# Kernel tuning notes

Measured on AMD Instinct MI355X. Metric: run time of the kernel, lower is better.

## Reference

```python
import jax, jax.numpy as jnp
import numpy as np

WIN = 25            # window size (win_h == win_w == 25)
DIM = 256           # channels
DIM_HEAD = 32
HEADS = DIM // DIM_HEAD   # 8
HIDDEN = int(DIM * 2.0)   # mlp_ratio = 2.0
EPS = 1e-5


def _rel_pos_indices(w=WIN):
    # replicates the buffer built in Attention.__init__
    pos = np.arange(w)
    gi, gj = np.meshgrid(pos, pos, indexing='ij')
    grid = np.stack([gi.ravel(), gj.ravel()], axis=-1)          # (w*w, 2)
    rel = grid[:, None, :] - grid[None, :, :] + (w - 1)          # (n, n, 2)
    return jnp.asarray(rel[..., 0] * (2 * w - 1) + rel[..., 1])  # (n, n) int


def setup_inputs() -> dict:
    key = jax.random.key(0)
    ks = jax.random.split(key, 8)
    s = 0.02
    d = DIM
    return {
        'x': jax.random.normal(ks[0], (2, d, 100, 100), jnp.float32),
        'w_qkv': jax.random.normal(ks[1], (3 * d, d), jnp.float32) * s,
        'w_out': jax.random.normal(ks[2], (d, d), jnp.float32) * s,
        'rel_bias_table': jax.random.normal(ks[3], ((2 * WIN - 1) ** 2, HEADS), jnp.float32) * s,
        'gamma2': jnp.ones((d,), jnp.float32),
        'beta2': jnp.zeros((d,), jnp.float32),
        'w1': jax.random.normal(ks[4], (HIDDEN, d), jnp.float32) * s,
        'b1': jnp.zeros((HIDDEN,), jnp.float32),
        'w2': jax.random.normal(ks[5], (d, HIDDEN), jnp.float32) * s,
        'b2': jnp.zeros((d,), jnp.float32),
    }


def _layernorm(x, g, b, eps=EPS):
    m = x.mean(-1, keepdims=True)
    v = ((x - m) ** 2).mean(-1, keepdims=True)
    return (x - m) / jnp.sqrt(v + eps) * g + b


def reference(x, w_qkv, w_out, rel_bias_table, gamma2, beta2, w1, b1, w2, b2):
    b, d, H, W = x.shape
    nh, nw = H // WIN, W // WIN
    h, dh = HEADS, DIM_HEAD
    scale = dh ** -0.5
    n = WIN * WIN

    # --- window partition: (b, d, H, W) -> (b*nh*nw, n, d) ---
    xw = x.reshape(b, d, nh, WIN, nw, WIN).transpose(0, 2, 4, 3, 5, 1)
    xw = xw.reshape(b * nh * nw, n, d)

    # --- windowed attention with relative-position bias (norm1 unused in source) ---
    qkv = xw @ w_qkv.T                         # (B, n, 3d)
    q, k, v = jnp.split(qkv, 3, axis=-1)
    split_heads = lambda t: t.reshape(t.shape[0], n, h, dh).transpose(0, 2, 1, 3)
    q = split_heads(q) * scale                 # (B, h, n, dh)
    k = split_heads(k)
    v = split_heads(v)

    sim = jnp.einsum('bhid,bhjd->bhij', q, k)  # (B, h, n, n)
    bias = rel_bias_table[_rel_pos_indices()]  # (n, n, h)
    sim = sim + bias.transpose(2, 0, 1)[None]
    attn = jax.nn.softmax(sim, axis=-1)
    out = jnp.einsum('bhij,bhjd->bhid', attn, v)            # (B, h, n, dh)
    out = out.transpose(0, 2, 1, 3).reshape(-1, n, d)        # head-major concat: (m d)
    out = out @ w_out.T                                      # (B, n, d)

    # --- un-partition: (b*nh*nw, n, d) -> (b, d, H, W) ---
    xa = out.reshape(b, nh, nw, WIN, WIN, d).transpose(0, 5, 1, 3, 2, 4)
    xa = xa.reshape(b, d, H, W)

    # --- norm2 + MLP + residual ---
    y = xa.transpose(0, 2, 3, 1).reshape(b, H * W, d)
    y = _layernorm(y, gamma2, beta2)
    y = jax.nn.gelu(y @ w1.T + b1, approximate=False) @ w2.T + b2
    y = y.reshape(b, H, W, d).transpose(0, 3, 1, 2)
    return x + y
```

## Files before the change

kernel.cpp:

```cpp
#include <hip/hip_runtime.h>


using f32x4 = __attribute__((ext_vector_type(4))) float;
using s16x8 = __attribute__((ext_vector_type(8))) short;

__device__ __forceinline__ ushort f2b(float f) {
  union { float f; unsigned u; } v; v.f = f;
  return (ushort)((v.u + 0x7FFFu + ((v.u >> 16) & 1u)) >> 16);
}
__device__ __forceinline__ ushort f2b_fast(float f) {
  union { float f; unsigned u; } v; v.f = f;
  return (ushort)((v.u + 0x8000u) >> 16);
}
__device__ __forceinline__ float b2f(ushort u) {
  union { unsigned u; float f; } v; v.u = ((unsigned)u) << 16; return v.f;
}
__device__ __forceinline__ float lo2f(unsigned w) {
  union { unsigned u; float f; } v; v.u = w << 16; return v.f;
}
__device__ __forceinline__ float hi2f(unsigned w) {
  union { unsigned u; float f; } v; v.u = w & 0xffff0000u; return v.f;
}

__device__ __forceinline__ void gld16(const void* g, void* l) {
  __builtin_amdgcn_global_load_lds((const __attribute__((address_space(1))) void*)g,
                                   (__attribute__((address_space(3))) void*)l, 16, 0, 0);
}

template<int KB>
__device__ __forceinline__ void gemm_core(const ushort* __restrict__ A, int lda,
                                          const ushort* __restrict__ B, int ldb,
                                          f32x4 acc[4][4]) {
  __shared__ ushort As[128 * 64];
  __shared__ ushort Bs[128 * 64];
  const int tid = threadIdx.x;
  const int lane = tid & 63;
  const int wv = tid >> 6;
  const int wr = (wv >> 1) * 64;
  const int wc = (wv & 1) * 64;
  const int srow = (lane >> 3);
  const int sg = ((lane & 7) ^ (srow & 7)) * 8;
  f32x4 zero = {0.f, 0.f, 0.f, 0.f};
#pragma unroll
  for (int mt = 0; mt < 4; ++mt)
#pragma unroll
    for (int nt = 0; nt < 4; ++nt) acc[mt][nt] = zero;

  for (int kb = 0; kb < KB; ++kb) {
#pragma unroll
    for (int j = 0; j < 4; ++j) {
      int r0 = wv * 32 + j * 8;
      int row = r0 + srow;
      gld16(A + row * lda + kb * 64 + sg, &As[r0 * 64]);
      gld16(B + row * ldb + kb * 64 + sg, &Bs[r0 * 64]);
    }
    __syncthreads();
#pragma unroll
    for (int ks = 0; ks < 2; ++ks) {
      s16x8 af[4], bfr[4];
      const int G = ks * 4 + (lane >> 4);
#pragma unroll
      for (int mt = 0; mt < 4; ++mt) {
        int row = wr + mt * 16 + (lane & 15);
        af[mt] = *(const s16x8*)&As[row * 64 + (G ^ (row & 7)) * 8];
      }
#pragma unroll
      for (int nt = 0; nt < 4; ++nt) {
        int row = wc + nt * 16 + (lane & 15);
        bfr[nt] = *(const s16x8*)&Bs[row * 64 + (G ^ (row & 7)) * 8];
      }
#pragma unroll
      for (int mt = 0; mt < 4; ++mt)
#pragma unroll
        for (int nt = 0; nt < 4; ++nt)
          acc[mt][nt] = __builtin_amdgcn_mfma_f32_16x16x32_bf16(af[mt], bfr[nt], acc[mt][nt], 0, 0, 0);
    }
    __syncthreads();
  }
}

__global__ __launch_bounds__(256) void k_prep(const float* __restrict__ x,
                                              const float* __restrict__ wqkv,
                                              const float* __restrict__ wout,
                                              const float* __restrict__ w1,
                                              const float* __restrict__ w2,
                                              const float* __restrict__ table,
                                              ushort* __restrict__ Xw,
                                              ushort* __restrict__ wqkvb,
                                              ushort* __restrict__ woutb,
                                              ushort* __restrict__ w1b,
                                              ushort* __restrict__ w2b,
                                              ushort* __restrict__ biasPh) {
  __shared__ ushort smem[64 * 264];
  const int bid = blockIdx.x, tid = threadIdx.x;
  if (bid < 320) {
    ushort (*Ls)[264] = (ushort(*)[264])smem;
    const int t0 = bid * 64;
    const int w = t0 / 640;
    const int tokbase = t0 - w * 640;
    const int b = w >> 4, wh = (w >> 2) & 3, ww = w & 3;
    for (int i = tid; i < 64 * 256; i += 256) {
      int c = i >> 6, tl = i & 63;
      int tok = tokbase + tl;
      ushort val = 0;
      if (tok < 625) {
        int ii = tok / 25, jj = tok - ii * 25;
        val = f2b(x[((b * 256 + c) * 100 + wh * 25 + ii) * 100 + ww * 25 + jj]);
      }
      Ls[tl][c] = val;
    }
    __syncthreads();
    for (int i = tid; i < 64 * 32; i += 256) {
      int tl = i >> 5, g = (i & 31) * 8;
      *(uint4*)(Xw + (t0 + tl) * 256 + g) = *(const uint4*)&Ls[tl][g];
    }
  } else if (bid < 832) {
    int v = (bid - 320) * 1024 + tid * 4;
    const float* src; ushort* dst; int off;
    if (v < 196608)      { src = wqkv; dst = wqkvb; off = v; }
    else if (v < 262144) { src = wout; dst = woutb; off = v - 196608; }
    else if (v < 393216) { src = w1;   dst = w1b;   off = v - 262144; }
    else                 { src = w2;   dst = w2b;   off = v - 393216; }
    float4 f = *(const float4*)(src + off);
    ushort4 u; u.x = f2b(f.x); u.y = f2b(f.y); u.z = f2b(f.z); u.w = f2b(f.w);
    *(ushort4*)(dst + off) = u;
  } else {
    float* tl = (float*)smem;
    const int q = bid - 832;
    const int h = q / 40, t = q - (q / 40) * 40;
    for (int i = tid; i < 2401; i += 256) tl[i] = table[i * 8 + h] * 1.4426950408889634f;
    __syncthreads();
    const int lane = tid >> 2, rr = tid & 3;
    const int quad = lane >> 4, cl = lane & 15;
    int row = t * 16 + quad * 4 + rr;
    int rowg = (row < 625) ? row : 0;
    const int ri = rowg / 25, ci = rowg - ri * 25;
    for (int cc = 0; cc < 4; ++cc)
      for (int cp = 0; cp < 5; ++cp)
#pragma unroll
        for (int codd = 0; codd < 2; ++codd) {
          int col = cc * 160 + (cp * 2 + codd) * 16 + cl;
          float v = -1e30f;
          if (col < 625) {
            int rj = col / 25, cj = col - rj * 25;
            v = tl[(ri - rj + 24) * 49 + (ci - cj + 24)];
          }
          biasPh[((((h * 40 + t) * 4 + cc) * 5 + cp) * 64 + lane) * 8 + codd * 4 + rr] = f2b(v);
        }
  }
}

__global__ __launch_bounds__(256) void k_qkv(const ushort* __restrict__ Xw,
                                             const ushort* __restrict__ Wb,
                                             ushort* __restrict__ Qb,
                                             ushort* __restrict__ Kb,
                                             ushort* __restrict__ Vb) {
  f32x4 acc[4][4];
  gemm_core<4>(Xw + blockIdx.x * 128 * 256, 256, Wb + blockIdx.y * 128 * 256, 256, acc);
  const int lane = threadIdx.x & 63, wv = threadIdx.x >> 6;
  const int wr = (wv >> 1) * 64, wc = (wv & 1) * 64;
  const float QSC = 0.17677669529663687f * 1.4426950408889634f;
#pragma unroll
  for (int mt = 0; mt < 4; ++mt) {
#pragma unroll
    for (int nt = 0; nt < 4; ++nt) {
      int n = blockIdx.y * 128 + wc + nt * 16 + (lane & 15);
      int which = n >> 8, h = (n >> 5) & 7, ch = n & 31;
      ushort* dst = which == 0 ? Qb : (which == 1 ? Kb : Vb);
      float sc = which == 0 ? QSC : 1.f;
#pragma unroll
      for (int r = 0; r < 4; ++r) {
        int m = blockIdx.x * 128 + wr + mt * 16 + (lane >> 4) * 4 + r;
        int w = m / 640, tok = m - w * 640;
        dst[(((w << 3) + h) * 640 + tok) * 32 + ch] = f2b_fast(acc[mt][nt][r] * sc);
      }
    }
  }
}

__global__ __launch_bounds__(256, 2) void k_attn(const ushort* __restrict__ Qb,
                                                 const ushort* __restrict__ Kb,
                                                 const ushort* __restrict__ Vb,
                                                 const ushort* __restrict__ biasPh,
                                                 ushort* __restrict__ AO) {
  __shared__ ushort Vt[32][646];
  __shared__ ushort Pw[4][16][164];
  const int tid = threadIdx.x;
  const int lane = tid & 63;
  const int wv = tid >> 6;
  const int quad = lane >> 4;
  const int cl = lane & 15;
  const int bid = blockIdx.x;
  const int tg = bid % 10;
  const int wh = bid / 10;
  const int h = wh & 7;
  const int win = wh >> 3;
  const ushort* Qg = Qb + (win * 8 + h) * 20480;
  const ushort* Kg = Kb + (win * 8 + h) * 20480;
  const ushort* Vg = Vb + (win * 8 + h) * 20480;

#pragma unroll
  for (int k = 0; k < 10; ++k) {
    int idx = tid + k * 256;
    int tok = idx >> 2, c0 = (idx & 3) * 8;
    ushort tmp[8];
    *(uint4*)tmp = *(const uint4*)(Vg + tok * 32 + c0);
#pragma unroll
    for (int j = 0; j < 8; ++j) Vt[c0 + j][tok] = tmp[j];
  }
  __syncthreads();

  const int t = tg * 4 + wv;
  const s16x8 qf = *(const s16x8*)(Qg + (t * 16 + cl) * 32 + quad * 8);
  const f32x4 zero = {0.f, 0.f, 0.f, 0.f};
  f32x4 o0 = zero, o1 = zero;
  float osum[4] = {0.f, 0.f, 0.f, 0.f};

  for (int cc = 0; cc < 4; ++cc) {
    f32x4 s[10];
#pragma unroll
    for (int c = 0; c < 10; ++c) {
      s16x8 kf = *(const s16x8*)(Kg + (cc * 160 + c * 16 + cl) * 32 + quad * 8);
      s[c] = __builtin_amdgcn_mfma_f32_16x16x32_bf16(qf, kf, zero, 0, 0, 0);
    }
    const ushort* bp = biasPh + (((h * 40 + t) * 4 + cc) * 5) * 512 + lane * 8;
#pragma unroll
    for (int cp = 0; cp < 5; ++cp) {
      s16x8 bb = *(const s16x8*)(bp + cp * 512);
      const unsigned* bw = (const unsigned*)&bb;
#pragma unroll
      for (int codd = 0; codd < 2; ++codd) {
        int c = cp * 2 + codd;
        unsigned w0 = bw[codd * 2], w1 = bw[codd * 2 + 1];
        s[c][0] += lo2f(w0); s[c][1] += hi2f(w0);
        s[c][2] += lo2f(w1); s[c][3] += hi2f(w1);
      }
    }
#pragma unroll
    for (int c = 0; c < 10; ++c)
#pragma unroll
      for (int r = 0; r < 4; ++r) {
        float p = exp2f(s[c][r]);
        osum[r] += p;
        Pw[wv][quad * 4 + r][c * 16 + cl] = f2b_fast(p);
      }
#pragma unroll
    for (int kc = 0; kc < 5; ++kc) {
      s16x8 pf = *(const s16x8*)&Pw[wv][cl][kc * 32 + quad * 8];
      s16x8 vf0 = *(const s16x8*)&Vt[cl][cc * 160 + kc * 32 + quad * 8];
      s16x8 vf1 = *(const s16x8*)&Vt[16 + cl][cc * 160 + kc * 32 + quad * 8];
      o0 = __builtin_amdgcn_mfma_f32_16x16x32_bf16(pf, vf0, o0, 0, 0, 0);
      o1 = __builtin_amdgcn_mfma_f32_16x16x32_bf16(pf, vf1, o1, 0, 0, 0);
    }
  }
#pragma unroll
  for (int r = 0; r < 4; ++r) {
    float ss = osum[r];
    ss += __shfl_xor(ss, 1, 64); ss += __shfl_xor(ss, 2, 64);
    ss += __shfl_xor(ss, 4, 64); ss += __shfl_xor(ss, 8, 64);
    float inv = 1.f / ss;
    int tok = t * 16 + quad * 4 + r;
    if (tok < 625) {
      int base = (win * 640 + tok) * 256 + h * 32;
      AO[base + cl] = f2b_fast(o0[r] * inv);
      AO[base + 16 + cl] = f2b_fast(o1[r] * inv);
    }
  }
}

__global__ __launch_bounds__(256, 2) void k_out_ln(const ushort* __restrict__ AO,
                                                   const ushort* __restrict__ Wb,
                                                   const float* __restrict__ gamma,
                                                   const float* __restrict__ beta,
                                                   ushort* __restrict__ Yn) {
  __shared__ ushort As[128 * 64];
  __shared__ ushort Bs[256 * 64];
  __shared__ float red[2][128][2];
  const int tid = threadIdx.x;
  const int lane = tid & 63;
  const int wv = tid >> 6;
  const int wr = (wv >> 1) * 64, wc = (wv & 1) * 128;
  const int quad = lane >> 4, cl = lane & 15;
  const int srow = lane >> 3;
  const int sg = ((lane & 7) ^ (srow & 7)) * 8;
  f32x4 zero = {0.f, 0.f, 0.f, 0.f};
  f32x4 acc[4][8];
#pragma unroll
  for (int mt = 0; mt < 4; ++mt)
#pragma unroll
    for (int nt = 0; nt < 8; ++nt) acc[mt][nt] = zero;

  const ushort* A = AO + blockIdx.x * 128 * 256;
  for (int kb = 0; kb < 4; ++kb) {
#pragma unroll
    for (int i = 0; i < 12; ++i) {
      int r0 = wv * 8 + i * 32;
      int row = r0 + srow;
      if (r0 < 128) gld16(A + row * 256 + kb * 64 + sg, &As[r0 * 64]);
      else          gld16(Wb + (row - 128) * 256 + kb * 64 + sg, &Bs[(r0 - 128) * 64]);
    }
    __syncthreads();
#pragma unroll
    for (int ks = 0; ks < 2; ++ks) {
      s16x8 af[4], bfr[8];
      const int G = ks * 4 + quad;
#pragma unroll
      for (int mt = 0; mt < 4; ++mt) {
        int row = wr + mt * 16 + cl;
        af[mt] = *(const s16x8*)&As[row * 64 + (G ^ (row & 7)) * 8];
      }
#pragma unroll
      for (int nt = 0; nt < 8; ++nt) {
        int row = wc + nt * 16 + cl;
        bfr[nt] = *(const s16x8*)&Bs[row * 64 + (G ^ (row & 7)) * 8];
      }
#pragma unroll
      for (int mt = 0; mt < 4; ++mt)
#pragma unroll
        for (int nt = 0; nt < 8; ++nt)
          acc[mt][nt] = __builtin_amdgcn_mfma_f32_16x16x32_bf16(af[mt], bfr[nt], acc[mt][nt], 0, 0, 0);
    }
    __syncthreads();
  }
#pragma unroll
  for (int mt = 0; mt < 4; ++mt)
#pragma unroll
    for (int r = 0; r < 4; ++r) {
      float s = 0.f, ss = 0.f;
#pragma unroll
      for (int nt = 0; nt < 8; ++nt) { float v = acc[mt][nt][r]; s += v; ss += v * v; }
      s += __shfl_xor(s, 1, 64); ss += __shfl_xor(ss, 1, 64);
      s += __shfl_xor(s, 2, 64); ss += __shfl_xor(ss, 2, 64);
      s += __shfl_xor(s, 4, 64); ss += __shfl_xor(ss, 4, 64);
      s += __shfl_xor(s, 8, 64); ss += __shfl_xor(ss, 8, 64);
      if (cl == 0) {
        int row = wr + mt * 16 + quad * 4 + r;
        red[wc >> 7][row][0] = s;
        red[wc >> 7][row][1] = ss;
      }
    }
  __syncthreads();
  float g[8], bt[8];
#pragma unroll
  for (int nt = 0; nt < 8; ++nt) { int n = wc + nt * 16 + cl; g[nt] = gamma[n]; bt[nt] = beta[n]; }
  const int m0 = blockIdx.x * 128;
#pragma unroll
  for (int mt = 0; mt < 4; ++mt)
#pragma unroll
    for (int r = 0; r < 4; ++r) {
      int row = wr + mt * 16 + quad * 4 + r;
      int m = m0 + row;
      int w = m / 640, tok = m - w * 640;
      if (tok < 625) {
        float sum = red[0][row][0] + red[1][row][0];
        float ssum = red[0][row][1] + red[1][row][1];
        float mean = sum * 0.00390625f;
        float var = ssum * 0.00390625f - mean * mean;
        float rstd = rsqrtf(var + 1e-5f);
        int b = w >> 4, whh = (w >> 2) & 3, www = w & 3;
        int ii = tok / 25, jj = tok - ii * 25;
        int p = (whh * 25 + ii) * 100 + www * 25 + jj;
        ushort* dst = Yn + (b * 10000 + p) * 256;
#pragma unroll
        for (int nt = 0; nt < 8; ++nt) {
          float v = (acc[mt][nt][r] - mean) * rstd * g[nt] + bt[nt];
          dst[wc + nt * 16 + cl] = f2b_fast(v);
        }
      }
    }
}

__global__ __launch_bounds__(256) void k_fc1(const ushort* __restrict__ Yn,
                                             const ushort* __restrict__ W1b,
                                             const float* __restrict__ b1,
                                             ushort* __restrict__ G) {
  f32x4 acc[4][4];
  gemm_core<4>(Yn + blockIdx.x * 128 * 256, 256, W1b + blockIdx.y * 128 * 256, 256, acc);
  const int lane = threadIdx.x & 63, wv = threadIdx.x >> 6;
  const int wr = (wv >> 1) * 64, wc = (wv & 1) * 64;
#pragma unroll
  for (int mt = 0; mt < 4; ++mt)
#pragma unroll
    for (int nt = 0; nt < 4; ++nt) {
      int n = blockIdx.y * 128 + wc + nt * 16 + (lane & 15);
      float bias = b1[n];
#pragma unroll
      for (int r = 0; r < 4; ++r) {
        int m = blockIdx.x * 128 + wr + mt * 16 + (lane >> 4) * 4 + r;
        float v = acc[mt][nt][r] + bias;
        v = 0.5f * v * (1.f + erff(v * 0.70710678118f));
        G[m * 512 + n] = f2b_fast(v);
      }
    }
}

__global__ __launch_bounds__(256) void k_fc2(const ushort* __restrict__ W2b,
                                             const ushort* __restrict__ G,
                                             const float* __restrict__ b2,
                                             const float* __restrict__ x,
                                             float* __restrict__ out) {
  f32x4 acc[4][4];
  gemm_core<8>(W2b + blockIdx.x * 128 * 512, 512, G + blockIdx.y * 128 * 512, 512, acc);
  const int lane = threadIdx.x & 63, wv = threadIdx.x >> 6;
  const int wr = (wv >> 1) * 64, wc = (wv & 1) * 64;
#pragma unroll
  for (int mt = 0; mt < 4; ++mt)
#pragma unroll
    for (int nt = 0; nt < 4; ++nt) {
      int t = blockIdx.y * 128 + wc + nt * 16 + (lane & 15);
      if (t < 20000) {
        int b = t / 10000, p = t - b * 10000;
#pragma unroll
        for (int r = 0; r < 4; ++r) {
          int c = blockIdx.x * 128 + wr + mt * 16 + (lane >> 4) * 4 + r;
          int idx = (b * 256 + c) * 10000 + p;
          out[idx] = x[idx] + acc[mt][nt][r] + b2[c];
        }
      }
    }
}

extern "C" void kernel_launch(void* const* d_in, const int* in_sizes, int n_in,
                              void* d_out, int out_size, void* d_ws, size_t ws_size,
                              hipStream_t stream) {
  const float* x     = (const float*)d_in[0];
  const float* wqkv  = (const float*)d_in[1];
  const float* wout  = (const float*)d_in[2];
  const float* bias  = (const float*)d_in[3];
  const float* gamma = (const float*)d_in[4];
  const float* beta  = (const float*)d_in[5];
  const float* w1    = (const float*)d_in[6];
  const float* b1    = (const float*)d_in[7];
  const float* w2    = (const float*)d_in[8];
  const float* b2    = (const float*)d_in[9];
  float* out = (float*)d_out;
  char* ws = (char*)d_ws;

  ushort* Xw    = (ushort*)(ws + 0);
  ushort* AO    = Xw;
  ushort* wqkvb = (ushort*)(ws + 10485760);
  ushort* woutb = (ushort*)(ws + 10878976);
  ushort* w1b   = (ushort*)(ws + 11010048);
  ushort* w2b   = (ushort*)(ws + 11272192);
  ushort* Qb    = (ushort*)(ws + 11534336);
  ushort* Kb    = (ushort*)(ws + 22020096);
  ushort* Vb    = (ushort*)(ws + 32505856);
  ushort* biasPh= (ushort*)(ws + 42991616);
  ushort* Yn    = (ushort*)(ws + 22020096);
  ushort* G     = (ushort*)(ws + 32505856);

  k_prep  <<<1152, 256, 0, stream>>>(x, wqkv, wout, w1, w2, bias,
                                     Xw, wqkvb, woutb, w1b, w2b, biasPh);
  k_qkv   <<<dim3(160, 6), 256, 0, stream>>>(Xw, wqkvb, Qb, Kb, Vb);
  k_attn  <<<2560, 256, 0, stream>>>(Qb, Kb, Vb, biasPh, AO);
  k_out_ln<<<160, 256, 0, stream>>>(AO, woutb, gamma, beta, Yn);
  k_fc1   <<<dim3(157, 4), 256, 0, stream>>>(Yn, w1b, b1, G);
  k_fc2   <<<dim3(2, 157), 256, 0, stream>>>(w2b, G, b2, x, out);
}
```

Before: 244.1 us.

## Write V transposed from QKV GEMM, drop LDS transpose in attention, shrink out-proj tile

```diff
diff --git a/kernel.cpp b/kernel.cpp
--- a/kernel.cpp
+++ b/kernel.cpp
@@ -154,36 +154,42 @@
                                              const ushort* __restrict__ Wb,
                                              ushort* __restrict__ Qb,
                                              ushort* __restrict__ Kb,
-                                             ushort* __restrict__ Vb) {
+                                             ushort* __restrict__ VbT) {
   f32x4 acc[4][4];
   gemm_core<4>(Xw + blockIdx.x * 128 * 256, 256, Wb + blockIdx.y * 128 * 256, 256, acc);
   const int lane = threadIdx.x & 63, wv = threadIdx.x >> 6;
   const int wr = (wv >> 1) * 64, wc = (wv & 1) * 64;
+  const int which = blockIdx.y >> 1;
   const float QSC = 0.17677669529663687f * 1.4426950408889634f;
 #pragma unroll
   for (int mt = 0; mt < 4; ++mt) {
 #pragma unroll
     for (int nt = 0; nt < 4; ++nt) {
       int n = blockIdx.y * 128 + wc + nt * 16 + (lane & 15);
-      int which = n >> 8, h = (n >> 5) & 7, ch = n & 31;
-      ushort* dst = which == 0 ? Qb : (which == 1 ? Kb : Vb);
-      float sc = which == 0 ? QSC : 1.f;
-#pragma unroll
-      for (int r = 0; r < 4; ++r) {
-        int m = blockIdx.x * 128 + wr + mt * 16 + (lane >> 4) * 4 + r;
-        int w = m / 640, tok = m - w * 640;
-        dst[(((w << 3) + h) * 640 + tok) * 32 + ch] = f2b_fast(acc[mt][nt][r] * sc);
-      }
-    }
-  }
-}
-
-__global__ __launch_bounds__(256, 2) void k_attn(const ushort* __restrict__ Qb,
+      int h = (n >> 5) & 7, ch = n & 31;
+      int m0 = blockIdx.x * 128 + wr + mt * 16 + (lane >> 4) * 4;
+      int w = m0 / 640, tok0 = m0 - w * 640;
+      if (which == 2) {
+        ushort4 pk;
+        pk.x = f2b_fast(acc[mt][nt][0]); pk.y = f2b_fast(acc[mt][nt][1]);
+        pk.z = f2b_fast(acc[mt][nt][2]); pk.w = f2b_fast(acc[mt][nt][3]);
+        *(ushort4*)(VbT + (((w << 3) + h) * 32 + ch) * 640 + tok0) = pk;
+      } else {
+        ushort* dst = which == 0 ? Qb : Kb;
+        float sc = which == 0 ? QSC : 1.f;
+#pragma unroll
+        for (int r = 0; r < 4; ++r)
+          dst[(((w << 3) + h) * 640 + tok0 + r) * 32 + ch] = f2b_fast(acc[mt][nt][r] * sc);
+      }
+    }
+  }
+}
+
+__global__ __launch_bounds__(256, 4) void k_attn(const ushort* __restrict__ Qb,
                                                  const ushort* __restrict__ Kb,
-                                                 const ushort* __restrict__ Vb,
+                                                 const ushort* __restrict__ VbT,
                                                  const ushort* __restrict__ biasPh,
                                                  ushort* __restrict__ AO) {
-  __shared__ ushort Vt[32][646];
   __shared__ ushort Pw[4][16][164];
   const int tid = threadIdx.x;
   const int lane = tid & 63;
@@ -191,24 +197,13 @@
   const int quad = lane >> 4;
   const int cl = lane & 15;
   const int bid = blockIdx.x;
-  const int tg = bid % 10;
-  const int wh = bid / 10;
-  const int h = wh & 7;
-  const int win = wh >> 3;
+  const int h = bid & 7;
+  const int rem = bid >> 3;
+  const int win = rem / 10;
+  const int tg = rem - win * 10;
   const ushort* Qg = Qb + (win * 8 + h) * 20480;
   const ushort* Kg = Kb + (win * 8 + h) * 20480;
-  const ushort* Vg = Vb + (win * 8 + h) * 20480;
-
-#pragma unroll
-  for (int k = 0; k < 10; ++k) {
-    int idx = tid + k * 256;
-    int tok = idx >> 2, c0 = (idx & 3) * 8;
-    ushort tmp[8];
-    *(uint4*)tmp = *(const uint4*)(Vg + tok * 32 + c0);
-#pragma unroll
-    for (int j = 0; j < 8; ++j) Vt[c0 + j][tok] = tmp[j];
-  }
-  __syncthreads();
+  const ushort* Vt = VbT + (win * 8 + h) * 20480;
 
   const int t = tg * 4 + wv;
   const s16x8 qf = *(const s16x8*)(Qg + (t * 16 + cl) * 32 + quad * 8);
@@ -247,8 +242,8 @@
 #pragma unroll
     for (int kc = 0; kc < 5; ++kc) {
       s16x8 pf = *(const s16x8*)&Pw[wv][cl][kc * 32 + quad * 8];
-      s16x8 vf0 = *(const s16x8*)&Vt[cl][cc * 160 + kc * 32 + quad * 8];
-      s16x8 vf1 = *(const s16x8*)&Vt[16 + cl][cc * 160 + kc * 32 + quad * 8];
+      s16x8 vf0 = *(const s16x8*)(Vt + cl * 640 + cc * 160 + kc * 32 + quad * 8);
+      s16x8 vf1 = *(const s16x8*)(Vt + (16 + cl) * 640 + cc * 160 + kc * 32 + quad * 8);
       o0 = __builtin_amdgcn_mfma_f32_16x16x32_bf16(pf, vf0, o0, 0, 0, 0);
       o1 = __builtin_amdgcn_mfma_f32_16x16x32_bf16(pf, vf1, o1, 0, 0, 0);
     }
@@ -273,39 +268,39 @@
                                                    const float* __restrict__ gamma,
                                                    const float* __restrict__ beta,
                                                    ushort* __restrict__ Yn) {
-  __shared__ ushort As[128 * 64];
+  __shared__ ushort As[64 * 64];
   __shared__ ushort Bs[256 * 64];
-  __shared__ float red[2][128][2];
+  __shared__ float red[2][64][2];
   const int tid = threadIdx.x;
   const int lane = tid & 63;
   const int wv = tid >> 6;
-  const int wr = (wv >> 1) * 64, wc = (wv & 1) * 128;
+  const int wr = (wv >> 1) * 32, wc = (wv & 1) * 128;
   const int quad = lane >> 4, cl = lane & 15;
   const int srow = lane >> 3;
   const int sg = ((lane & 7) ^ (srow & 7)) * 8;
   f32x4 zero = {0.f, 0.f, 0.f, 0.f};
-  f32x4 acc[4][8];
-#pragma unroll
-  for (int mt = 0; mt < 4; ++mt)
+  f32x4 acc[2][8];
+#pragma unroll
+  for (int mt = 0; mt < 2; ++mt)
 #pragma unroll
     for (int nt = 0; nt < 8; ++nt) acc[mt][nt] = zero;
 
-  const ushort* A = AO + blockIdx.x * 128 * 256;
+  const ushort* A = AO + blockIdx.x * 64 * 256;
   for (int kb = 0; kb < 4; ++kb) {
 #pragma unroll
-    for (int i = 0; i < 12; ++i) {
-      int r0 = wv * 8 + i * 32;
+    for (int i = 0; i < 10; ++i) {
+      int r0 = (wv + i * 4) * 8;
       int row = r0 + srow;
-      if (r0 < 128) gld16(A + row * 256 + kb * 64 + sg, &As[r0 * 64]);
-      else          gld16(Wb + (row - 128) * 256 + kb * 64 + sg, &Bs[(r0 - 128) * 64]);
+      if (r0 < 64) gld16(A + row * 256 + kb * 64 + sg, &As[r0 * 64]);
+      else         gld16(Wb + (row - 64) * 256 + kb * 64 + sg, &Bs[(r0 - 64) * 64]);
     }
     __syncthreads();
 #pragma unroll
     for (int ks = 0; ks < 2; ++ks) {
-      s16x8 af[4], bfr[8];
+      s16x8 af[2], bfr[8];
       const int G = ks * 4 + quad;
 #pragma unroll
-      for (int mt = 0; mt < 4; ++mt) {
+      for (int mt = 0; mt < 2; ++mt) {
         int row = wr + mt * 16 + cl;
         af[mt] = *(const s16x8*)&As[row * 64 + (G ^ (row & 7)) * 8];
       }
@@ -315,7 +310,7 @@
         bfr[nt] = *(const s16x8*)&Bs[row * 64 + (G ^ (row & 7)) * 8];
       }
 #pragma unroll
-      for (int mt = 0; mt < 4; ++mt)
+      for (int mt = 0; mt < 2; ++mt)
 #pragma unroll
         for (int nt = 0; nt < 8; ++nt)
           acc[mt][nt] = __builtin_amdgcn_mfma_f32_16x16x32_bf16(af[mt], bfr[nt], acc[mt][nt], 0, 0, 0);
@@ -323,7 +318,7 @@
     __syncthreads();
   }
 #pragma unroll
-  for (int mt = 0; mt < 4; ++mt)
+  for (int mt = 0; mt < 2; ++mt)
 #pragma unroll
     for (int r = 0; r < 4; ++r) {
       float s = 0.f, ss = 0.f;
@@ -343,9 +338,9 @@
   float g[8], bt[8];
 #pragma unroll
   for (int nt = 0; nt < 8; ++nt) { int n = wc + nt * 16 + cl; g[nt] = gamma[n]; bt[nt] = beta[n]; }
-  const int m0 = blockIdx.x * 128;
-#pragma unroll
-  for (int mt = 0; mt < 4; ++mt)
+  const int m0 = blockIdx.x * 64;
+#pragma unroll
+  for (int mt = 0; mt < 2; ++mt)
 #pragma unroll
     for (int r = 0; r < 4; ++r) {
       int row = wr + mt * 16 + quad * 4 + r;
@@ -444,16 +439,16 @@
   ushort* w2b   = (ushort*)(ws + 11272192);
   ushort* Qb    = (ushort*)(ws + 11534336);
   ushort* Kb    = (ushort*)(ws + 22020096);
-  ushort* Vb    = (ushort*)(ws + 32505856);
+  ushort* VbT   = (ushort*)(ws + 32505856);
   ushort* biasPh= (ushort*)(ws + 42991616);
   ushort* Yn    = (ushort*)(ws + 22020096);
   ushort* G     = (ushort*)(ws + 32505856);
 
   k_prep  <<<1152, 256, 0, stream>>>(x, wqkv, wout, w1, w2, bias,
                                      Xw, wqkvb, woutb, w1b, w2b, biasPh);
-  k_qkv   <<<dim3(160, 6), 256, 0, stream>>>(Xw, wqkvb, Qb, Kb, Vb);
-  k_attn  <<<2560, 256, 0, stream>>>(Qb, Kb, Vb, biasPh, AO);
-  k_out_ln<<<160, 256, 0, stream>>>(AO, woutb, gamma, beta, Yn);
+  k_qkv   <<<dim3(160, 6), 256, 0, stream>>>(Xw, wqkvb, Qb, Kb, VbT);
+  k_attn  <<<2560, 256, 0, stream>>>(Qb, Kb, VbT, biasPh, AO);
+  k_out_ln<<<320, 256, 0, stream>>>(AO, woutb, gamma, beta, Yn);
   k_fc1   <<<dim3(157, 4), 256, 0, stream>>>(Yn, w1b, b1, G);
   k_fc2   <<<dim3(2, 157), 256, 0, stream>>>(w2b, G, b2, x, out);
 }
```

Result: slower. 251.5 us (+3.0%).
